# Kernel optimization log

Hardware: AMD Instinct MI355X
Metric: run time of the kernel (lower is better)

## Reference

```python
import jax, jax.numpy as jnp
import numpy as np

NEG_BIG = -9.0e15  # matches torch zero_vec constant


def setup_inputs() -> dict:
    key = jax.random.key(0)
    k1, k2, k3, k4, k5 = jax.random.split(key, 5)
    B, N, D_IN, D_HID, D_OUT = 4, 4096, 128, 64, 128
    h = jax.random.normal(k1, (B, N, D_IN), dtype=jnp.float32)
    adj = jax.random.randint(k2, (N, N), 0, 2, dtype=jnp.int32)
    Ws = jax.random.normal(k3, (D_IN, D_HID), dtype=jnp.float32) * (1.414 / np.sqrt(D_IN))
    Wt = jax.random.normal(k4, (D_IN, D_HID), dtype=jnp.float32) * (1.414 / np.sqrt(D_IN))
    Wc = jax.random.normal(k5, (D_IN, D_OUT), dtype=jnp.float32) * np.sqrt(2.0 / D_IN)
    return {"h": h, "adj": adj, "Ws": Ws, "Wt": Wt, "Wc": Wc}


def reference(h, adj, Ws, Wt, Wc):
    # h: [B,N,D_in], adj: [N,N] broadcast over batch
    Whs = jnp.matmul(h, Ws)                     # [B,N,H]
    Wht = jnp.matmul(h, Wt)                     # [B,N,H]
    e = jnp.einsum('bnh,bmh->bnm', Whs, Wht)    # [B,N,N] dense scores
    z = jnp.where(adj > 0, e, NEG_BIG)          # adjacency mask
    alpha = jax.nn.softmax(z, axis=-1)          # [B,N,N]
    Whc = jnp.matmul(h, Wc)                     # [B,N,D_out]
    h_prime = jnp.matmul(alpha, Whc)            # [B,N,D_out]
    return h_prime
```

## Files before the change

kernel.cpp:

```cpp
#include <hip/hip_runtime.h>
#include <hip/hip_bf16.h>

#define NTOK 4096
#define BATCH 4
#define DIN 128
#define DHID 64
#define DOUT 128
#define NWRD (NTOK / 32)
#define SPLIT 4
#define ITERS (NTOK / SPLIT / 64)
#define NEG_BIG -9.0e15f

typedef short short8 __attribute__((ext_vector_type(8)));
typedef float floatx4 __attribute__((ext_vector_type(4)));

static __device__ __forceinline__ unsigned short f2bf(float f) {
    unsigned int u = __builtin_bit_cast(unsigned int, f);
    u = (u + 0x7fffu + ((u >> 16) & 1u)) >> 16;
    return (unsigned short)u;
}
static __device__ __forceinline__ float bf2f(unsigned short s) {
    unsigned int u = ((unsigned int)s) << 16;
    return __builtin_bit_cast(float, u);
}

static __device__ __forceinline__ floatx4 mfma16(short8 a, short8 b, floatx4 c) {
    return __builtin_amdgcn_mfma_f32_16x16x32_bf16(a, b, c, 0, 0, 0);
}

__global__ __launch_bounds__(256) void pack_adj_kernel(const int* __restrict__ adj,
                                                       unsigned int* __restrict__ bits) {
    int w = blockIdx.x * 256 + threadIdx.x;
    const int4* p = reinterpret_cast<const int4*>(adj) + (size_t)w * 8;
    unsigned int m = 0;
#pragma unroll
    for (int i = 0; i < 8; ++i) {
        int4 v = p[i];
        m |= (v.x > 0 ? 1u : 0u) << (4 * i + 0);
        m |= (v.y > 0 ? 1u : 0u) << (4 * i + 1);
        m |= (v.z > 0 ? 1u : 0u) << (4 * i + 2);
        m |= (v.w > 0 ? 1u : 0u) << (4 * i + 3);
    }
    bits[w] = m;
}

__global__ __launch_bounds__(256) void conv_w_kernel(const float* __restrict__ Ws,
                                                     const float* __restrict__ Wt,
                                                     const float* __restrict__ Wc,
                                                     unsigned short* __restrict__ WT_hi,
                                                     unsigned short* __restrict__ WT_lo) {
    int idx = blockIdx.x * 256 + threadIdx.x;
    int k = idx >> 8, col = idx & 255;
    float w;
    if (col < 64) w = Ws[k * DHID + col];
    else if (col < 128) w = Wt[k * DHID + (col - 64)];
    else w = Wc[k * DOUT + (col - 128)];
    unsigned short hi = f2bf(w);
    WT_hi[col * DIN + k] = hi;
    if (col < 128) WT_lo[col * DIN + k] = f2bf(w - bf2f(hi));
}

__global__ __launch_bounds__(256) void prep_kernel(const float* __restrict__ h,
                                                   const unsigned short* __restrict__ WT_hi,
                                                   const unsigned short* __restrict__ WT_lo,
                                                   unsigned short* __restrict__ Whs_hi,
                                                   unsigned short* __restrict__ Whs_lo,
                                                   unsigned short* __restrict__ Wht_hi,
                                                   unsigned short* __restrict__ Wht_lo,
                                                   unsigned short* __restrict__ WhcT) {
    int tid = threadIdx.x;
    int b = blockIdx.y;
    int w = tid >> 6, lane = tid & 63, lg = lane >> 4, lc = lane & 15;
    int n0 = blockIdx.x * 16;
    const float* hrow = h + (size_t)(b * NTOK + n0 + lc) * DIN;

    short8 ah[4], al[4];
#pragma unroll
    for (int ks = 0; ks < 4; ++ks) {
        float4 f0 = *reinterpret_cast<const float4*>(hrow + ks * 32 + lg * 8);
        float4 f1 = *reinterpret_cast<const float4*>(hrow + ks * 32 + lg * 8 + 4);
        float x[8] = {f0.x, f0.y, f0.z, f0.w, f1.x, f1.y, f1.z, f1.w};
        short8 hh, ll;
#pragma unroll
        for (int j = 0; j < 8; ++j) {
            unsigned short hb = f2bf(x[j]);
            hh[j] = (short)hb;
            ll[j] = (short)f2bf(x[j] - bf2f(hb));
        }
        ah[ks] = hh;
        al[ks] = ll;
    }

#pragma unroll
    for (int ci = 0; ci < 4; ++ci) {
        int ct = w * 4 + ci;
        int col = ct * 16 + lc;
        const unsigned short* bbase = WT_hi + (size_t)col * DIN;
        const unsigned short* lbase = WT_lo + (size_t)col * DIN;
        floatx4 acc = {0.f, 0.f, 0.f, 0.f};
#pragma unroll
        for (int ks = 0; ks < 4; ++ks) {
            short8 bh = *reinterpret_cast<const short8*>(bbase + ks * 32 + lg * 8);
            acc = mfma16(ah[ks], bh, acc);
            if (w < 2) {
                short8 bl = *reinterpret_cast<const short8*>(lbase + ks * 32 + lg * 8);
                acc = mfma16(ah[ks], bl, acc);
                acc = mfma16(al[ks], bh, acc);
            }
        }
        int nr = n0 + 4 * lg;
        if (w == 0) {
#pragma unroll
            for (int r = 0; r < 4; ++r) {
                float v = acc[r];
                unsigned short hb = f2bf(v);
                size_t o = (size_t)(b * NTOK + nr + r) * DHID + col;
                Whs_hi[o] = hb;
                Whs_lo[o] = f2bf(v - bf2f(hb));
            }
        } else if (w == 1) {
#pragma unroll
            for (int r = 0; r < 4; ++r) {
                float v = acc[r];
                unsigned short hb = f2bf(v);
                size_t o = (size_t)(b * NTOK + nr + r) * DHID + (col - 64);
                Wht_hi[o] = hb;
                Wht_lo[o] = f2bf(v - bf2f(hb));
            }
        } else {
            unsigned int p01 = (unsigned int)f2bf(acc[0]) | ((unsigned int)f2bf(acc[1]) << 16);
            unsigned int p23 = (unsigned int)f2bf(acc[2]) | ((unsigned int)f2bf(acc[3]) << 16);
            unsigned int* dst =
                reinterpret_cast<unsigned int*>(&WhcT[(size_t)(b * DOUT + col - 128) * NTOK + nr]);
            dst[0] = p01;
            dst[1] = p23;
        }
    }
}

__global__ __launch_bounds__(256) void attn_kernel(const unsigned short* __restrict__ Whs_hi,
                                                   const unsigned short* __restrict__ Whs_lo,
                                                   const unsigned short* __restrict__ Wht_hi,
                                                   const unsigned short* __restrict__ Wht_lo,
                                                   const unsigned short* __restrict__ WhcT,
                                                   const unsigned int* __restrict__ bits,
                                                   unsigned short* __restrict__ po,
                                                   float* __restrict__ pm,
                                                   float* __restrict__ pl) {
    __shared__ unsigned short Kh_lds[64][72];
    __shared__ unsigned short Kl_lds[64][72];
    __shared__ unsigned short V_lds[128][72];
    __shared__ unsigned short P_lds[4][16][72];

    int tid = threadIdx.x;
    int b = blockIdx.y;
    int split = blockIdx.z;
    int kbase = split * (NTOK / SPLIT);
    int w = tid >> 6, lane = tid & 63, lg = lane >> 4, lc = lane & 15;
    int q0 = blockIdx.x * 64 + w * 16;

    const unsigned short* qrowH = Whs_hi + (size_t)(b * NTOK + q0 + lc) * DHID;
    const unsigned short* qrowL = Whs_lo + (size_t)(b * NTOK + q0 + lc) * DHID;
    short8 qh0 = *reinterpret_cast<const short8*>(qrowH + lg * 8);
    short8 qh1 = *reinterpret_cast<const short8*>(qrowH + 32 + lg * 8);
    short8 ql0 = *reinterpret_cast<const short8*>(qrowL + lg * 8);
    short8 ql1 = *reinterpret_cast<const short8*>(qrowL + 32 + lg * 8);

    floatx4 o[8];
#pragma unroll
    for (int dt = 0; dt < 8; ++dt) o[dt] = (floatx4){0.f, 0.f, 0.f, 0.f};
    float m[4], l[4];
#pragma unroll
    for (int r = 0; r < 4; ++r) { m[r] = NEG_BIG; l[r] = 0.f; }

    int kkey = tid >> 2, koff = (tid & 3) * 16;
    int vd = tid >> 1, voff = (tid & 1) * 32;

    short8 krH0, krH1, krL0, krL1, vr0, vr1, vr2, vr3;
    unsigned int mw0[4], mw1[4];

    {
        int kb = kbase;
        const unsigned short* ksrcH = Wht_hi + (size_t)(b * NTOK + kb + kkey) * DHID + koff;
        const unsigned short* ksrcL = Wht_lo + (size_t)(b * NTOK + kb + kkey) * DHID + koff;
        krH0 = *reinterpret_cast<const short8*>(ksrcH);
        krH1 = *reinterpret_cast<const short8*>(ksrcH + 8);
        krL0 = *reinterpret_cast<const short8*>(ksrcL);
        krL1 = *reinterpret_cast<const short8*>(ksrcL + 8);
        const unsigned short* vsrc = WhcT + (size_t)(b * DOUT + vd) * NTOK + kb + voff;
        vr0 = *reinterpret_cast<const short8*>(vsrc);
        vr1 = *reinterpret_cast<const short8*>(vsrc + 8);
        vr2 = *reinterpret_cast<const short8*>(vsrc + 16);
        vr3 = *reinterpret_cast<const short8*>(vsrc + 24);
#pragma unroll
        for (int r = 0; r < 4; ++r) {
            int n = q0 + 4 * lg + r;
            mw0[r] = bits[n * NWRD + (kb >> 5)];
            mw1[r] = bits[n * NWRD + (kb >> 5) + 1];
        }
    }

    for (int it = 0; it < ITERS; ++it) {
        __syncthreads();
        *reinterpret_cast<short8*>(&Kh_lds[kkey][koff]) = krH0;
        *reinterpret_cast<short8*>(&Kh_lds[kkey][koff + 8]) = krH1;
        *reinterpret_cast<short8*>(&Kl_lds[kkey][koff]) = krL0;
        *reinterpret_cast<short8*>(&Kl_lds[kkey][koff + 8]) = krL1;
        *reinterpret_cast<short8*>(&V_lds[vd][voff]) = vr0;
        *reinterpret_cast<short8*>(&V_lds[vd][voff + 8]) = vr1;
        *reinterpret_cast<short8*>(&V_lds[vd][voff + 16]) = vr2;
        *reinterpret_cast<short8*>(&V_lds[vd][voff + 24]) = vr3;
        __syncthreads();

        floatx4 s[4];
#pragma unroll
        for (int kc = 0; kc < 4; ++kc) {
            short8 kh0 = *reinterpret_cast<const short8*>(&Kh_lds[kc * 16 + lc][lg * 8]);
            short8 kh1 = *reinterpret_cast<const short8*>(&Kh_lds[kc * 16 + lc][32 + lg * 8]);
            short8 kl0 = *reinterpret_cast<const short8*>(&Kl_lds[kc * 16 + lc][lg * 8]);
            short8 kl1 = *reinterpret_cast<const short8*>(&Kl_lds[kc * 16 + lc][32 + lg * 8]);
            floatx4 acc = {0.f, 0.f, 0.f, 0.f};
            acc = mfma16(qh0, kh0, acc);
            acc = mfma16(qh1, kh1, acc);
            acc = mfma16(ql0, kh0, acc);
            acc = mfma16(ql1, kh1, acc);
            acc = mfma16(qh0, kl0, acc);
            acc = mfma16(qh1, kl1, acc);
            s[kc] = acc;
        }

#pragma unroll
        for (int r = 0; r < 4; ++r) {
#pragma unroll
            for (int kc = 0; kc < 4; ++kc) {
                unsigned int word = (kc & 2) ? mw1[r] : mw0[r];
                int bit = ((kc & 1) * 16) + lc;
                if (!((word >> bit) & 1u)) s[kc][r] = NEG_BIG;
            }
        }

        if (it + 1 < ITERS) {
            int kb = kbase + (it + 1) * 64;
            const unsigned short* ksrcH = Wht_hi + (size_t)(b * NTOK + kb + kkey) * DHID + koff;
            const unsigned short* ksrcL = Wht_lo + (size_t)(b * NTOK + kb + kkey) * DHID + koff;
            krH0 = *reinterpret_cast<const short8*>(ksrcH);
            krH1 = *reinterpret_cast<const short8*>(ksrcH + 8);
            krL0 = *reinterpret_cast<const short8*>(ksrcL);
            krL1 = *reinterpret_cast<const short8*>(ksrcL + 8);
            const unsigned short* vsrc = WhcT + (size_t)(b * DOUT + vd) * NTOK + kb + voff;
            vr0 = *reinterpret_cast<const short8*>(vsrc);
            vr1 = *reinterpret_cast<const short8*>(vsrc + 8);
            vr2 = *reinterpret_cast<const short8*>(vsrc + 16);
            vr3 = *reinterpret_cast<const short8*>(vsrc + 24);
#pragma unroll
            for (int r = 0; r < 4; ++r) {
                int n = q0 + 4 * lg + r;
                mw0[r] = bits[n * NWRD + (kb >> 5)];
                mw1[r] = bits[n * NWRD + (kb >> 5) + 1];
            }
        }

        float mn[4], sc[4], rs[4];
#pragma unroll
        for (int r = 0; r < 4; ++r) {
            float vm = fmaxf(fmaxf(s[0][r], s[1][r]), fmaxf(s[2][r], s[3][r]));
            vm = fmaxf(vm, __shfl_xor(vm, 1));
            vm = fmaxf(vm, __shfl_xor(vm, 2));
            vm = fmaxf(vm, __shfl_xor(vm, 4));
            vm = fmaxf(vm, __shfl_xor(vm, 8));
            float mnr = fmaxf(m[r], vm);
            sc[r] = __expf(m[r] - mnr);
            mn[r] = mnr;
            m[r] = mnr;
            rs[r] = 0.f;
        }
#pragma unroll
        for (int kc = 0; kc < 4; ++kc)
#pragma unroll
            for (int r = 0; r < 4; ++r) {
                float p = __expf(s[kc][r] - mn[r]);
                s[kc][r] = p;
                rs[r] += p;
            }
#pragma unroll
        for (int r = 0; r < 4; ++r) {
            float t = rs[r];
            t += __shfl_xor(t, 1);
            t += __shfl_xor(t, 2);
            t += __shfl_xor(t, 4);
            t += __shfl_xor(t, 8);
            l[r] = l[r] * sc[r] + t;
        }
#pragma unroll
        for (int dt = 0; dt < 8; ++dt)
#pragma unroll
            for (int r = 0; r < 4; ++r) o[dt][r] *= sc[r];

#pragma unroll
        for (int kc = 0; kc < 4; ++kc)
#pragma unroll
            for (int r = 0; r < 4; ++r)
                P_lds[w][4 * lg + r][kc * 16 + lc] = f2bf(s[kc][r]);
        asm volatile("s_waitcnt lgkmcnt(0)" ::: "memory");
        __builtin_amdgcn_sched_barrier(0);
        short8 pa0 = *reinterpret_cast<const short8*>(&P_lds[w][lc][lg * 8]);
        short8 pa1 = *reinterpret_cast<const short8*>(&P_lds[w][lc][32 + lg * 8]);

#pragma unroll
        for (int dt = 0; dt < 8; ++dt) {
            short8 vf0 = *reinterpret_cast<const short8*>(&V_lds[dt * 16 + lc][lg * 8]);
            o[dt] = mfma16(pa0, vf0, o[dt]);
        }
#pragma unroll
        for (int dt = 0; dt < 8; ++dt) {
            short8 vf1 = *reinterpret_cast<const short8*>(&V_lds[dt * 16 + lc][32 + lg * 8]);
            o[dt] = mfma16(pa1, vf1, o[dt]);
        }
    }

#pragma unroll
    for (int r = 0; r < 4; ++r) {
        size_t row = (size_t)(split * BATCH + b) * NTOK + q0 + 4 * lg + r;
        unsigned short* prow = po + row * DOUT;
#pragma unroll
        for (int dt = 0; dt < 8; ++dt) prow[dt * 16 + lc] = f2bf(o[dt][r]);
        if (lc == 0) {
            pm[row] = m[r];
            pl[row] = l[r];
        }
    }
}

__global__ __launch_bounds__(256) void merge_kernel(const unsigned short* __restrict__ po,
                                                    const float* __restrict__ pm,
                                                    const float* __restrict__ pl,
                                                    float* __restrict__ out) {
    int idx = blockIdx.x * 256 + threadIdx.x;
    int d = idx & (DOUT - 1);
    size_t bn = (size_t)(idx >> 7);
    const size_t BN = (size_t)BATCH * NTOK;

    float ms[SPLIT];
#pragma unroll
    for (int s = 0; s < SPLIT; ++s) ms[s] = pm[s * BN + bn];
    float M = ms[0];
#pragma unroll
    for (int s = 1; s < SPLIT; ++s) M = fmaxf(M, ms[s]);
    float L = 0.f, acc = 0.f;
#pragma unroll
    for (int s = 0; s < SPLIT; ++s) {
        float e = __expf(ms[s] - M);
        L += pl[s * BN + bn] * e;
        acc += bf2f(po[(s * BN + bn) * DOUT + d]) * e;
    }
    out[idx] = acc / L;
}

extern "C" void kernel_launch(void* const* d_in, const int* in_sizes, int n_in,
                              void* d_out, int out_size, void* d_ws, size_t ws_size,
                              hipStream_t stream) {
    const float* h   = (const float*)d_in[0];
    const int*   adj = (const int*)d_in[1];
    const float* Ws  = (const float*)d_in[2];
    const float* Wt  = (const float*)d_in[3];
    const float* Wc  = (const float*)d_in[4];
    float* out = (float*)d_out;

    size_t nq = (size_t)BATCH * NTOK * DHID;
    unsigned short* Whs_hi = (unsigned short*)d_ws;
    unsigned short* Whs_lo = Whs_hi + nq;
    unsigned short* Wht_hi = Whs_lo + nq;
    unsigned short* Wht_lo = Wht_hi + nq;
    unsigned short* WhcT   = Wht_lo + nq;
    unsigned int*   bits   = (unsigned int*)(WhcT + (size_t)BATCH * DOUT * NTOK);
    unsigned short* WT_hi  = (unsigned short*)(bits + (size_t)NTOK * NWRD);
    unsigned short* WT_lo  = WT_hi + 256 * DIN;
    unsigned short* po     = WT_lo + 128 * DIN;
    float*          pm     = (float*)(po + (size_t)SPLIT * BATCH * NTOK * DOUT);
    float*          pl     = pm + (size_t)SPLIT * BATCH * NTOK;

    pack_adj_kernel<<<dim3(NTOK * NWRD / 256), dim3(256), 0, stream>>>(adj, bits);
    conv_w_kernel<<<dim3(128), dim3(256), 0, stream>>>(Ws, Wt, Wc, WT_hi, WT_lo);
    prep_kernel<<<dim3(NTOK / 16, BATCH), dim3(256), 0, stream>>>(
        h, WT_hi, WT_lo, Whs_hi, Whs_lo, Wht_hi, Wht_lo, WhcT);
    attn_kernel<<<dim3(NTOK / 64, BATCH, SPLIT), dim3(256), 0, stream>>>(
        Whs_hi, Whs_lo, Wht_hi, Wht_lo, WhcT, bits, po, pm, pl);
    merge_kernel<<<dim3(BATCH * NTOK * DOUT / 256), dim3(256), 0, stream>>>(po, pm, pl, out);
}
```

Before: 230.2 us.

## Transpose score MFMA so P stays in registers, drop P LDS round-trip

The QK^T MFMA operands are swapped so each lane owns one query row. Softmax max and sum now reduce within a lane plus two cross-group shuffles instead of four per row. The probabilities are packed to bf16 in registers with v_cvt_pk_bf16_f32 and fed straight to the PV MFMA, which removes the P shared-memory write, wait and read. V is stored to LDS in a permuted key order to match that register layout. It also adds s_setprio around the MFMA sections and a launch-bounds occupancy hint, which could raise register pressure or introduce permutation mistakes.

```diff
diff --git a/kernel.cpp b/kernel.cpp
--- a/kernel.cpp
+++ b/kernel.cpp
@@ -12,6 +12,7 @@
 #define NEG_BIG -9.0e15f
 
 typedef short short8 __attribute__((ext_vector_type(8)));
+typedef short short4v __attribute__((ext_vector_type(4)));
 typedef float floatx4 __attribute__((ext_vector_type(4)));
 
 static __device__ __forceinline__ unsigned short f2bf(float f) {
@@ -22,6 +23,11 @@
 static __device__ __forceinline__ float bf2f(unsigned short s) {
     unsigned int u = ((unsigned int)s) << 16;
     return __builtin_bit_cast(float, u);
+}
+static __device__ __forceinline__ unsigned int pk2(float lo, float hi) {
+    unsigned int r;
+    asm("v_cvt_pk_bf16_f32 %0, %1, %2" : "=v"(r) : "v"(lo), "v"(hi));
+    return r;
 }
 
 static __device__ __forceinline__ floatx4 mfma16(short8 a, short8 b, floatx4 c) {
@@ -138,29 +144,29 @@
     }
 }
 
-__global__ __launch_bounds__(256) void attn_kernel(const unsigned short* __restrict__ Whs_hi,
-                                                   const unsigned short* __restrict__ Whs_lo,
-                                                   const unsigned short* __restrict__ Wht_hi,
-                                                   const unsigned short* __restrict__ Wht_lo,
-                                                   const unsigned short* __restrict__ WhcT,
-                                                   const unsigned int* __restrict__ bits,
-                                                   unsigned short* __restrict__ po,
-                                                   float* __restrict__ pm,
-                                                   float* __restrict__ pl) {
+__global__ __launch_bounds__(256, 4) void attn_kernel(const unsigned short* __restrict__ Whs_hi,
+                                                      const unsigned short* __restrict__ Whs_lo,
+                                                      const unsigned short* __restrict__ Wht_hi,
+                                                      const unsigned short* __restrict__ Wht_lo,
+                                                      const unsigned short* __restrict__ WhcT,
+                                                      const unsigned int* __restrict__ bits,
+                                                      unsigned short* __restrict__ po,
+                                                      float* __restrict__ pm,
+                                                      float* __restrict__ pl) {
     __shared__ unsigned short Kh_lds[64][72];
     __shared__ unsigned short Kl_lds[64][72];
     __shared__ unsigned short V_lds[128][72];
-    __shared__ unsigned short P_lds[4][16][72];
 
     int tid = threadIdx.x;
     int b = blockIdx.y;
     int split = blockIdx.z;
     int kbase = split * (NTOK / SPLIT);
-    int w = tid >> 6, lane = tid & 63, lg = lane >> 4, lc = lane & 15;
-    int q0 = blockIdx.x * 64 + w * 16;
-
-    const unsigned short* qrowH = Whs_hi + (size_t)(b * NTOK + q0 + lc) * DHID;
-    const unsigned short* qrowL = Whs_lo + (size_t)(b * NTOK + q0 + lc) * DHID;
+    int lane = tid & 63, lg = lane >> 4, lc = lane & 15;
+    int q0 = blockIdx.x * 64 + (tid >> 6) * 16;
+    int n = q0 + lc;
+
+    const unsigned short* qrowH = Whs_hi + (size_t)(b * NTOK + n) * DHID;
+    const unsigned short* qrowL = Whs_lo + (size_t)(b * NTOK + n) * DHID;
     short8 qh0 = *reinterpret_cast<const short8*>(qrowH + lg * 8);
     short8 qh1 = *reinterpret_cast<const short8*>(qrowH + 32 + lg * 8);
     short8 ql0 = *reinterpret_cast<const short8*>(qrowL + lg * 8);
@@ -169,15 +175,13 @@
     floatx4 o[8];
 #pragma unroll
     for (int dt = 0; dt < 8; ++dt) o[dt] = (floatx4){0.f, 0.f, 0.f, 0.f};
-    float m[4], l[4];
-#pragma unroll
-    for (int r = 0; r < 4; ++r) { m[r] = NEG_BIG; l[r] = 0.f; }
+    float m = NEG_BIG, l = 0.f;
 
     int kkey = tid >> 2, koff = (tid & 3) * 16;
-    int vd = tid >> 1, voff = (tid & 1) * 32;
+    int vd = tid >> 1, va = tid & 1;
 
     short8 krH0, krH1, krL0, krL1, vr0, vr1, vr2, vr3;
-    unsigned int mw0[4], mw1[4];
+    unsigned int mw0, mw1;
 
     {
         int kb = kbase;
@@ -187,17 +191,13 @@
         krH1 = *reinterpret_cast<const short8*>(ksrcH + 8);
         krL0 = *reinterpret_cast<const short8*>(ksrcL);
         krL1 = *reinterpret_cast<const short8*>(ksrcL + 8);
-        const unsigned short* vsrc = WhcT + (size_t)(b * DOUT + vd) * NTOK + kb + voff;
+        const unsigned short* vsrc = WhcT + (size_t)(b * DOUT + vd) * NTOK + kb + va * 32;
         vr0 = *reinterpret_cast<const short8*>(vsrc);
         vr1 = *reinterpret_cast<const short8*>(vsrc + 8);
         vr2 = *reinterpret_cast<const short8*>(vsrc + 16);
         vr3 = *reinterpret_cast<const short8*>(vsrc + 24);
-#pragma unroll
-        for (int r = 0; r < 4; ++r) {
-            int n = q0 + 4 * lg + r;
-            mw0[r] = bits[n * NWRD + (kb >> 5)];
-            mw1[r] = bits[n * NWRD + (kb >> 5) + 1];
-        }
+        mw0 = bits[n * NWRD + (kb >> 5)];
+        mw1 = bits[n * NWRD + (kb >> 5) + 1];
     }
 
     for (int it = 0; it < ITERS; ++it) {
@@ -206,13 +206,22 @@
         *reinterpret_cast<short8*>(&Kh_lds[kkey][koff + 8]) = krH1;
         *reinterpret_cast<short8*>(&Kl_lds[kkey][koff]) = krL0;
         *reinterpret_cast<short8*>(&Kl_lds[kkey][koff + 8]) = krL1;
-        *reinterpret_cast<short8*>(&V_lds[vd][voff]) = vr0;
-        *reinterpret_cast<short8*>(&V_lds[vd][voff + 8]) = vr1;
-        *reinterpret_cast<short8*>(&V_lds[vd][voff + 16]) = vr2;
-        *reinterpret_cast<short8*>(&V_lds[vd][voff + 24]) = vr3;
+        {
+            int sb = va * 32;
+            const short8 vv[4] = {vr0, vr1, vr2, vr3};
+#pragma unroll
+            for (int j = 0; j < 4; ++j) {
+                short4v lo4 = {vv[j][0], vv[j][1], vv[j][2], vv[j][3]};
+                short4v hi4 = {vv[j][4], vv[j][5], vv[j][6], vv[j][7]};
+                int s0 = sb + 16 * (j & 1) + 4 * (j >> 1);
+                *reinterpret_cast<short4v*>(&V_lds[vd][s0]) = lo4;
+                *reinterpret_cast<short4v*>(&V_lds[vd][s0 + 8]) = hi4;
+            }
+        }
         __syncthreads();
 
         floatx4 s[4];
+        __builtin_amdgcn_s_setprio(1);
 #pragma unroll
         for (int kc = 0; kc < 4; ++kc) {
             short8 kh0 = *reinterpret_cast<const short8*>(&Kh_lds[kc * 16 + lc][lg * 8]);
@@ -220,21 +229,22 @@
             short8 kl0 = *reinterpret_cast<const short8*>(&Kl_lds[kc * 16 + lc][lg * 8]);
             short8 kl1 = *reinterpret_cast<const short8*>(&Kl_lds[kc * 16 + lc][32 + lg * 8]);
             floatx4 acc = {0.f, 0.f, 0.f, 0.f};
-            acc = mfma16(qh0, kh0, acc);
-            acc = mfma16(qh1, kh1, acc);
-            acc = mfma16(ql0, kh0, acc);
-            acc = mfma16(ql1, kh1, acc);
-            acc = mfma16(qh0, kl0, acc);
-            acc = mfma16(qh1, kl1, acc);
+            acc = mfma16(kh0, qh0, acc);
+            acc = mfma16(kh1, qh1, acc);
+            acc = mfma16(kh0, ql0, acc);
+            acc = mfma16(kh1, ql1, acc);
+            acc = mfma16(kl0, qh0, acc);
+            acc = mfma16(kl1, qh1, acc);
             s[kc] = acc;
         }
-
-#pragma unroll
-        for (int r = 0; r < 4; ++r) {
-#pragma unroll
-            for (int kc = 0; kc < 4; ++kc) {
-                unsigned int word = (kc & 2) ? mw1[r] : mw0[r];
-                int bit = ((kc & 1) * 16) + lc;
+        __builtin_amdgcn_s_setprio(0);
+
+#pragma unroll
+        for (int kc = 0; kc < 4; ++kc) {
+            unsigned int word = (kc & 2) ? mw1 : mw0;
+#pragma unroll
+            for (int r = 0; r < 4; ++r) {
+                int bit = 16 * (kc & 1) + 4 * lg + r;
                 if (!((word >> bit) & 1u)) s[kc][r] = NEG_BIG;
             }
         }
@@ -247,65 +257,55 @@
             krH1 = *reinterpret_cast<const short8*>(ksrcH + 8);
             krL0 = *reinterpret_cast<const short8*>(ksrcL);
             krL1 = *reinterpret_cast<const short8*>(ksrcL + 8);
-            const unsigned short* vsrc = WhcT + (size_t)(b * DOUT + vd) * NTOK + kb + voff;
+            const unsigned short* vsrc = WhcT + (size_t)(b * DOUT + vd) * NTOK + kb + va * 32;
             vr0 = *reinterpret_cast<const short8*>(vsrc);
             vr1 = *reinterpret_cast<const short8*>(vsrc + 8);
             vr2 = *reinterpret_cast<const short8*>(vsrc + 16);
             vr3 = *reinterpret_cast<const short8*>(vsrc + 24);
+            mw0 = bits[n * NWRD + (kb >> 5)];
+            mw1 = bits[n * NWRD + (kb >> 5) + 1];
+        }
+
+        float vm = s[0][0];
+#pragma unroll
+        for (int kc = 0; kc < 4; ++kc)
+#pragma unroll
+            for (int r = 0; r < 4; ++r) vm = fmaxf(vm, s[kc][r]);
+        vm = fmaxf(vm, __shfl_xor(vm, 16));
+        vm = fmaxf(vm, __shfl_xor(vm, 32));
+        float mn = fmaxf(m, vm);
+        float sc = __expf(m - mn);
+        m = mn;
+        float rs = 0.f;
+#pragma unroll
+        for (int kc = 0; kc < 4; ++kc)
 #pragma unroll
             for (int r = 0; r < 4; ++r) {
-                int n = q0 + 4 * lg + r;
-                mw0[r] = bits[n * NWRD + (kb >> 5)];
-                mw1[r] = bits[n * NWRD + (kb >> 5) + 1];
-            }
-        }
-
-        float mn[4], sc[4], rs[4];
-#pragma unroll
-        for (int r = 0; r < 4; ++r) {
-            float vm = fmaxf(fmaxf(s[0][r], s[1][r]), fmaxf(s[2][r], s[3][r]));
-            vm = fmaxf(vm, __shfl_xor(vm, 1));
-            vm = fmaxf(vm, __shfl_xor(vm, 2));
-            vm = fmaxf(vm, __shfl_xor(vm, 4));
-            vm = fmaxf(vm, __shfl_xor(vm, 8));
-            float mnr = fmaxf(m[r], vm);
-            sc[r] = __expf(m[r] - mnr);
-            mn[r] = mnr;
-            m[r] = mnr;
-            rs[r] = 0.f;
-        }
-#pragma unroll
-        for (int kc = 0; kc < 4; ++kc)
-#pragma unroll
-            for (int r = 0; r < 4; ++r) {
-                float p = __expf(s[kc][r] - mn[r]);
+                float p = __expf(s[kc][r] - mn);
                 s[kc][r] = p;
-                rs[r] += p;
-            }
-#pragma unroll
-        for (int r = 0; r < 4; ++r) {
-            float t = rs[r];
-            t += __shfl_xor(t, 1);
-            t += __shfl_xor(t, 2);
-            t += __shfl_xor(t, 4);
-            t += __shfl_xor(t, 8);
-            l[r] = l[r] * sc[r] + t;
-        }
+                rs += p;
+            }
+        rs += __shfl_xor(rs, 16);
+        rs += __shfl_xor(rs, 32);
+        l = l * sc + rs;
+
+        float sc4[4];
+#pragma unroll
+        for (int r = 0; r < 4; ++r) sc4[r] = __shfl(sc, (lane & 48) + 4 * lg + r);
 #pragma unroll
         for (int dt = 0; dt < 8; ++dt)
 #pragma unroll
-            for (int r = 0; r < 4; ++r) o[dt][r] *= sc[r];
-
-#pragma unroll
-        for (int kc = 0; kc < 4; ++kc)
-#pragma unroll
-            for (int r = 0; r < 4; ++r)
-                P_lds[w][4 * lg + r][kc * 16 + lc] = f2bf(s[kc][r]);
-        asm volatile("s_waitcnt lgkmcnt(0)" ::: "memory");
-        __builtin_amdgcn_sched_barrier(0);
-        short8 pa0 = *reinterpret_cast<const short8*>(&P_lds[w][lc][lg * 8]);
-        short8 pa1 = *reinterpret_cast<const short8*>(&P_lds[w][lc][32 + lg * 8]);
-
+            for (int r = 0; r < 4; ++r) o[dt][r] *= sc4[r];
+
+        unsigned int pw[8];
+        pw[0] = pk2(s[0][0], s[0][1]); pw[1] = pk2(s[0][2], s[0][3]);
+        pw[2] = pk2(s[1][0], s[1][1]); pw[3] = pk2(s[1][2], s[1][3]);
+        pw[4] = pk2(s[2][0], s[2][1]); pw[5] = pk2(s[2][2], s[2][3]);
+        pw[6] = pk2(s[3][0], s[3][1]); pw[7] = pk2(s[3][2], s[3][3]);
+        short8 pa0 = __builtin_bit_cast(short8, *reinterpret_cast<uint4*>(&pw[0]));
+        short8 pa1 = __builtin_bit_cast(short8, *reinterpret_cast<uint4*>(&pw[4]));
+
+        __builtin_amdgcn_s_setprio(1);
 #pragma unroll
         for (int dt = 0; dt < 8; ++dt) {
             short8 vf0 = *reinterpret_cast<const short8*>(&V_lds[dt * 16 + lc][lg * 8]);
@@ -316,8 +316,16 @@
             short8 vf1 = *reinterpret_cast<const short8*>(&V_lds[dt * 16 + lc][32 + lg * 8]);
             o[dt] = mfma16(pa1, vf1, o[dt]);
         }
-    }
-
+        __builtin_amdgcn_s_setprio(0);
+    }
+
+    float m4[4], l4[4];
+#pragma unroll
+    for (int r = 0; r < 4; ++r) {
+        int src = (lane & 48) + 4 * lg + r;
+        m4[r] = __shfl(m, src);
+        l4[r] = __shfl(l, src);
+    }
 #pragma unroll
     for (int r = 0; r < 4; ++r) {
         size_t row = (size_t)(split * BATCH + b) * NTOK + q0 + 4 * lg + r;
@@ -325,8 +333,8 @@
 #pragma unroll
         for (int dt = 0; dt < 8; ++dt) prow[dt * 16 + lc] = f2bf(o[dt][r]);
         if (lc == 0) {
-            pm[row] = m[r];
-            pl[row] = l[r];
+            pm[row] = m4[r];
+            pl[row] = l4[r];
         }
     }
 }
```

After: 222.0 us. -3.6%, faster.
